# Optimization experiments

Hardware: AMD Instinct MI355X
Metric: run time of the kernel (lower is better)

The kernel has to match this reference:

```python
import jax, jax.numpy as jnp
import numpy as np

B, T, C = 8, 2048, 768
HEAD = 64
NUM_REL = 2048


def setup_inputs() -> dict:
    key = jax.random.key(0)
    k1, k2, k3, k4, k5 = jax.random.split(key, 5)
    input_tensor = jax.random.normal(k1, (B, T, C), dtype=jnp.float32)
    # torch Linear(C, HEAD, bias=False): y = x @ W.T, W:[HEAD,C]; store as [C,HEAD]
    Wq = jax.random.normal(k2, (C, HEAD), dtype=jnp.float32) * (C ** -0.5)
    Wk = jax.random.normal(k3, (C, HEAD), dtype=jnp.float32) * (C ** -0.5)
    Wv = jax.random.normal(k4, (C, HEAD), dtype=jnp.float32) * (C ** -0.5)
    bias_table = jax.random.normal(k5, (NUM_REL, 1), dtype=jnp.float32)
    return {"input_tensor": input_tensor, "Wq": Wq, "Wk": Wk, "Wv": Wv, "bias_table": bias_table}


def reference(input_tensor, Wq, Wk, Wv, bias_table):
    Bsz, Tlen, _ = input_tensor.shape
    q = input_tensor @ Wq  # [B,T,H]
    k = input_tensor @ Wk
    v = input_tensor @ Wv
    scale = q.shape[-1] ** -0.5
    scores = jnp.einsum('bqh,bkh->bqk', q, k) * scale  # [B,T,T]
    # relative position bias: clamp(i - j, 0, NUM_REL-1)
    qpos = jnp.arange(Tlen)[:, None]
    kpos = jnp.arange(Tlen)[None, :]
    rel = jnp.clip(qpos - kpos, 0, bias_table.shape[0] - 1)
    bias = bias_table[rel, 0]  # [T,T]
    scores = scores + bias
    causal = kpos <= qpos  # True where allowed
    scores = jnp.where(causal, scores, -jnp.inf)
    attn = jax.nn.softmax(scores, axis=-1)
    return jnp.einsum('bqk,bkh->bqh', attn, v)
```

## Files before the change

### kernel.cpp

```cpp
#include <hip/hip_runtime.h>
#include <hip/hip_bf16.h>

typedef __attribute__((ext_vector_type(8))) short bf16x8;
typedef __attribute__((ext_vector_type(4))) short short4v;
typedef __attribute__((ext_vector_type(4))) float f32x4;

#define B_SZ 8
#define T_SZ 2048
#define C_SZ 768
#define H_SZ 64

__device__ __forceinline__ short f2bs(float f){
  __hip_bfloat16 h = __float2bfloat16(f);
  short s; __builtin_memcpy(&s, &h, 2); return s;
}
__device__ __forceinline__ f32x4 vmax4(f32x4 a, f32x4 b){
  f32x4 r; r[0]=fmaxf(a[0],b[0]); r[1]=fmaxf(a[1],b[1]);
  r[2]=fmaxf(a[2],b[2]); r[3]=fmaxf(a[3],b[3]); return r;
}
__device__ __forceinline__ void gload16(const void* g, void* l){
  __builtin_amdgcn_global_load_lds(
    (const __attribute__((address_space(1))) unsigned int*)g,
    (__attribute__((address_space(3))) unsigned int*)l, 16, 0, 0);
}

__global__ __launch_bounds__(256) void prep_wt(const float* __restrict__ Wq, const float* __restrict__ Wk,
                        const float* __restrict__ Wv, const float* __restrict__ bias,
                        short* __restrict__ Wt, float* __restrict__ bsc){
  int tid = threadIdx.x;
  if (blockIdx.x >= 36){
    int i = (blockIdx.x - 36)*256 + tid;
    bsc[i] = bias[i] * 1.44269504f;
    return;
  }
  __shared__ float tile[64][65];
  int mat = blockIdx.x / 12, kblk = blockIdx.x % 12;
  const float* W = (mat == 0) ? Wq : (mat == 1 ? Wk : Wv);
  int k0 = kblk * 64;
  int r = tid >> 2, cq = (tid & 3) * 16;
  #pragma unroll
  for (int i = 0; i < 4; ++i){
    float4 v = *reinterpret_cast<const float4*>(&W[(k0 + r)*H_SZ + cq + i*4]);
    tile[r][cq + i*4 + 0] = v.x; tile[r][cq + i*4 + 1] = v.y;
    tile[r][cq + i*4 + 2] = v.z; tile[r][cq + i*4 + 3] = v.w;
  }
  __syncthreads();
  int n = tid >> 2, kq = (tid & 3) * 16;
  bf16x8 o0, o1;
  #pragma unroll
  for (int e = 0; e < 8; ++e){
    o0[e] = f2bs(tile[kq + e][n]);
    o1[e] = f2bs(tile[kq + 8 + e][n]);
  }
  *reinterpret_cast<bf16x8*>(&Wt[(mat*64 + n)*C_SZ + k0 + kq])     = o0;
  *reinterpret_cast<bf16x8*>(&Wt[(mat*64 + n)*C_SZ + k0 + kq + 8]) = o1;
}

__global__ __launch_bounds__(512, 2) void qkv_gemm(const float* __restrict__ x, const short* __restrict__ Wt,
                         short* __restrict__ qb, short* __restrict__ kb, short* __restrict__ vT){
  __shared__ float As[2][2048];
  __shared__ short Bs[2][12288];
  int tid = threadIdx.x;
  int wv = tid >> 6, lane = tid & 63, lhi = lane >> 4, llo = lane & 15;
  int wm = wv >> 2, wn = wv & 3;
  long R0 = (long)blockIdx.x * 32;

  int srow = tid >> 4;
  int schunk = (tid & 15) ^ (srow & 7);
  const float* gsrcA = &x[(R0 + srow)*C_SZ + schunk*4];
  float* ldstA = &As[0][wv*256];

  int bn = tid >> 3;
  int bc = (tid & 7) ^ (bn & 7);
  const short* gsrcB0 = &Wt[(  0 + bn)*C_SZ + bc*8];
  const short* gsrcB1 = &Wt[( 64 + bn)*C_SZ + bc*8];
  const short* gsrcB2 = &Wt[(128 + bn)*C_SZ + bc*8];
  short* ldstB = &Bs[0][wv*512];

  f32x4 acc[3];
  #pragma unroll
  for (int j = 0; j < 3; ++j) acc[j] = (f32x4){0.f,0.f,0.f,0.f};

  int rr = wm*16 + llo;
  int r7 = rr & 7, lhi2 = lhi*2;
  int c0 = ((lhi2    ) ^ r7) << 2;
  int c1 = ((lhi2 + 1) ^ r7) << 2;
  int c2 = ((lhi2 + 8) ^ r7) << 2;
  int c3 = ((lhi2 + 9) ^ r7) << 2;
  int nrow[3];
  #pragma unroll
  for (int j = 0; j < 3; ++j) nrow[j] = (wn*48 + j*16 + llo)*64;
  int llo7 = llo & 7;
  int bo0 = ((    lhi) ^ llo7)*8;
  int bo1 = ((4 + lhi) ^ llo7)*8;

#define STAGE(T, BUF) { \
    gload16(gsrcA  + (T)*64, ldstA + (BUF)*2048); \
    gload16(gsrcB0 + (T)*64, ldstB + (BUF)*12288); \
    gload16(gsrcB1 + (T)*64, ldstB + (BUF)*12288 + 4096); \
    gload16(gsrcB2 + (T)*64, ldstB + (BUF)*12288 + 8192); }

  STAGE(0, 0);
  __syncthreads();

  for (int t = 0; t < 12; ++t){
    int cb = t & 1;
    if (t < 11) STAGE(t + 1, cb ^ 1);
    const float* Ar = &As[cb][rr*64];
    f32x4 a0 = *reinterpret_cast<const f32x4*>(Ar + c0);
    f32x4 a1 = *reinterpret_cast<const f32x4*>(Ar + c1);
    f32x4 a2 = *reinterpret_cast<const f32x4*>(Ar + c2);
    f32x4 a3 = *reinterpret_cast<const f32x4*>(Ar + c3);
    bf16x8 af0, af1;
    #pragma unroll
    for (int e = 0; e < 4; ++e){
      af0[e]   = f2bs(a0[e]); af0[4+e] = f2bs(a1[e]);
      af1[e]   = f2bs(a2[e]); af1[4+e] = f2bs(a3[e]);
    }
    const short* Br = &Bs[cb][0];
    #pragma unroll
    for (int j = 0; j < 3; ++j){
      bf16x8 b0 = *reinterpret_cast<const bf16x8*>(Br + nrow[j] + bo0);
      bf16x8 b1 = *reinterpret_cast<const bf16x8*>(Br + nrow[j] + bo1);
      acc[j] = __builtin_amdgcn_mfma_f32_16x16x32_bf16(af0, b0, acc[j], 0, 0, 0);
      acc[j] = __builtin_amdgcn_mfma_f32_16x16x32_bf16(af1, b1, acc[j], 0, 0, 0);
    }
    __syncthreads();
  }
#undef STAGE

  long mbase = R0 + wm*16 + lhi*4;
  #pragma unroll
  for (int j = 0; j < 3; ++j){
    int n = wn*48 + j*16 + llo;
    int mat = n >> 6, c = n & 63;
    if (mat == 2){
      long b = mbase >> 11, t = mbase & 2047;
      short4v p;
      #pragma unroll
      for (int reg = 0; reg < 4; ++reg) p[reg] = f2bs(acc[j][reg]);
      *reinterpret_cast<short4v*>(&vT[(b*H_SZ + c)*T_SZ + t]) = p;
    } else {
      short* dst = (mat == 0) ? qb : kb;
      #pragma unroll
      for (int reg = 0; reg < 4; ++reg)
        dst[(mbase + reg)*H_SZ + c] = f2bs(acc[j][reg]);
    }
  }
}

__global__ __launch_bounds__(512, 2) void attn_fwd(const short* __restrict__ qb, const short* __restrict__ kb,
                        const short* __restrict__ vT, const float* __restrict__ bsc,
                        float* __restrict__ out){
  __shared__ float bias_s[2048];
  __shared__ float pool[8][1040];
  __shared__ float m_part[8][16];
  __shared__ float l_part[8][16];

  int tid = threadIdx.x;
  for (int i = tid; i < 2048; i += 512) bias_s[i] = bsc[i];

  int wv = tid >> 6, lane = tid & 63, lhi = lane >> 4, llo = lane & 15;
  int g = wv >> 2, ws = wv & 3;
  int b = blockIdx.x & 7, jj = blockIdx.x >> 3;
  int qt = g ? (127 - jj) : jj;
  int q0 = qt * 16;
  int q = q0 + llo;

  const short* qrow = &qb[((long)(b*T_SZ + q))*H_SZ + lhi*8];
  bf16x8 qf0 = *reinterpret_cast<const bf16x8*>(qrow);
  bf16x8 qf1 = *reinterpret_cast<const bf16x8*>(qrow + 32);
  const short* kbase = kb + (long)b*T_SZ*H_SZ;
  const short* vbase = vT + (long)b*H_SZ*T_SZ;
  short* Pw = (short*)&pool[wv][0];
  __syncthreads();

  float m_r = -1e30f, l_r = 0.f;
  f32x4 o[4];
  #pragma unroll
  for (int df = 0; df < 4; ++df) o[df] = (f32x4){0.f,0.f,0.f,0.f};

  int nkt = (qt >> 2) + 1;
  for (int kt = ws; kt < nkt; kt += 4){
    int kv0 = kt * 64;
    bf16x8 kf0[4], kf1[4];
    #pragma unroll
    for (int f = 0; f < 4; ++f){
      const short* kr = kbase + (long)(kv0 + f*16 + llo)*H_SZ + lhi*8;
      kf0[f] = *reinterpret_cast<const bf16x8*>(kr);
      kf1[f] = *reinterpret_cast<const bf16x8*>(kr + 32);
    }
    f32x4 s[4];
    #pragma unroll
    for (int f = 0; f < 4; ++f){
      f32x4 t = (f32x4){0.f,0.f,0.f,0.f};
      t = __builtin_amdgcn_mfma_f32_16x16x32_bf16(kf0[f], qf0, t, 0, 0, 0);
      t = __builtin_amdgcn_mfma_f32_16x16x32_bf16(kf1[f], qf1, t, 0, 0, 0);
      s[f] = t;
    }
    bf16x8 vf0[4], vf1[4];
    #pragma unroll
    for (int d = 0; d < 4; ++d){
      const short* vr = vbase + (long)(d*16 + llo)*T_SZ + kv0 + lhi*8;
      vf0[d] = *reinterpret_cast<const bf16x8*>(vr);
      vf1[d] = *reinterpret_cast<const bf16x8*>(vr + 32);
    }
    #pragma unroll
    for (int f = 0; f < 4; ++f)
      #pragma unroll
      for (int rg = 0; rg < 4; ++rg){
        int kv = kv0 + f*16 + lhi*4 + rg;
        int rel = q - kv;
        float bv = bias_s[rel > 0 ? rel : 0];
        s[f][rg] = (rel >= 0) ? fmaf(s[f][rg], 0.18033688f, bv) : -1e30f;
      }
    f32x4 tm = vmax4(vmax4(s[0], s[1]), vmax4(s[2], s[3]));
    float pmax = fmaxf(fmaxf(tm[0], tm[1]), fmaxf(tm[2], tm[3]));
    pmax = fmaxf(pmax, __shfl_xor(pmax, 16));
    pmax = fmaxf(pmax, __shfl_xor(pmax, 32));
    bool keep = __all(pmax <= m_r + 8.0f);
    if (!keep){
      float mnew = fmaxf(m_r, pmax);
      float corr = exp2f(m_r - mnew);
      m_r = mnew;
      l_r *= corr;
      #pragma unroll
      for (int df = 0; df < 4; ++df) o[df] = o[df] * corr;
    }
    #pragma unroll
    for (int f = 0; f < 4; ++f)
      #pragma unroll
      for (int rg = 0; rg < 4; ++rg)
        s[f][rg] = exp2f(s[f][rg] - m_r);
    f32x4 va = (s[0] + s[1]) + (s[2] + s[3]);
    float rs = (va[0] + va[1]) + (va[2] + va[3]);
    rs += __shfl_xor(rs, 16);
    rs += __shfl_xor(rs, 32);
    l_r += rs;
    #pragma unroll
    for (int f = 0; f < 4; ++f){
      short4v pk;
      #pragma unroll
      for (int rg = 0; rg < 4; ++rg) pk[rg] = f2bs(s[f][rg]);
      *reinterpret_cast<short4v*>(&Pw[llo*72 + f*16 + lhi*4]) = pk;
    }
    bf16x8 pb0 = *reinterpret_cast<const bf16x8*>(&Pw[llo*72 + lhi*8]);
    bf16x8 pb1 = *reinterpret_cast<const bf16x8*>(&Pw[llo*72 + 32 + lhi*8]);
    #pragma unroll
    for (int df = 0; df < 4; ++df){
      o[df] = __builtin_amdgcn_mfma_f32_16x16x32_bf16(vf0[df], pb0, o[df], 0, 0, 0);
      o[df] = __builtin_amdgcn_mfma_f32_16x16x32_bf16(vf1[df], pb1, o[df], 0, 0, 0);
    }
  }

  #pragma unroll
  for (int df = 0; df < 4; ++df)
    #pragma unroll
    for (int rg = 0; rg < 4; ++rg)
      pool[wv][llo*65 + df*16 + lhi*4 + rg] = o[df][rg];
  if (lhi == 0){ m_part[wv][llo] = m_r; l_part[wv][llo] = l_r; }
  __syncthreads();

  int g2 = tid >> 8, r2 = tid & 255;
  int d = r2 & 63, q4 = r2 >> 6;
  int qt2 = g2 ? (127 - jj) : jj;
  long obase = ((long)(b*T_SZ + qt2*16))*H_SZ;
  #pragma unroll
  for (int i = 0; i < 4; ++i){
    int qq = q4*4 + i;
    float mstar = m_part[g2*4][qq];
    #pragma unroll
    for (int w = 1; w < 4; ++w) mstar = fmaxf(mstar, m_part[g2*4 + w][qq]);
    float lsum = 0.f, osum = 0.f;
    #pragma unroll
    for (int w = 0; w < 4; ++w){
      float sc = exp2f(m_part[g2*4 + w][qq] - mstar);
      lsum += l_part[g2*4 + w][qq] * sc;
      osum += pool[g2*4 + w][qq*65 + d] * sc;
    }
    out[obase + (long)qq*H_SZ + d] = osum / lsum;
  }
}

extern "C" void kernel_launch(void* const* d_in, const int* in_sizes, int n_in,
                              void* d_out, int out_size, void* d_ws, size_t ws_size,
                              hipStream_t stream){
  const float* x    = (const float*)d_in[0];
  const float* Wq   = (const float*)d_in[1];
  const float* Wk   = (const float*)d_in[2];
  const float* Wv   = (const float*)d_in[3];
  const float* bias = (const float*)d_in[4];
  float* out = (float*)d_out;

  const size_t NTOK = (size_t)B_SZ * T_SZ * H_SZ;
  short* qb = (short*)d_ws;
  short* kb = qb + NTOK;
  short* vT = kb + NTOK;
  short* Wt = vT + NTOK;
  float* bsc = (float*)(Wt + 192*C_SZ);

  prep_wt<<<44, 256, 0, stream>>>(Wq, Wk, Wv, bias, Wt, bsc);
  qkv_gemm<<<512, 512, 0, stream>>>(x, Wt, qb, kb, vT);
  attn_fwd<<<512, 512, 0, stream>>>(qb, kb, vT, bsc, out);
}
```

Measured before the change: 62.32 us.

## Process paired query tiles in every wave, sharing K/V loads across both tiles

Each wave now computes both the light (jj) and heavy (127-jj) query tiles together, so every K and V fragment loaded is used for two MFMA streams instead of one. All 8 waves split the key range of the longer tile, which replaces the earlier fixed 4+4 wave split and spreads the causal work more evenly. The row-sum shuffles are deferred to the final merge by keeping per-lane partial sums, and launch bounds ask for 4 blocks per CU. The cost is extra accumulator registers, which may spill under the tighter register limit, plus two serialized merge passes with added block barriers.

```diff
diff --git a/kernel.cpp b/kernel.cpp
--- a/kernel.cpp
+++ b/kernel.cpp
@@ -149,137 +149,137 @@
   }
 }
 
-__global__ __launch_bounds__(512, 2) void attn_fwd(const short* __restrict__ qb, const short* __restrict__ kb,
+__global__ __launch_bounds__(512, 4) void attn_fwd(const short* __restrict__ qb, const short* __restrict__ kb,
                         const short* __restrict__ vT, const float* __restrict__ bsc,
                         float* __restrict__ out){
   __shared__ float bias_s[2048];
-  __shared__ float pool[8][1040];
+  __shared__ short P_lds[8][2][1152];
   __shared__ float m_part[8][16];
-  __shared__ float l_part[8][16];
+  __shared__ float l_part[8][4][16];
+  float* OP = (float*)&P_lds[0][0][0];
 
   int tid = threadIdx.x;
   for (int i = tid; i < 2048; i += 512) bias_s[i] = bsc[i];
 
   int wv = tid >> 6, lane = tid & 63, lhi = lane >> 4, llo = lane & 15;
-  int g = wv >> 2, ws = wv & 3;
   int b = blockIdx.x & 7, jj = blockIdx.x >> 3;
-  int qt = g ? (127 - jj) : jj;
-  int q0 = qt * 16;
-  int q = q0 + llo;
-
-  const short* qrow = &qb[((long)(b*T_SZ + q))*H_SZ + lhi*8];
-  bf16x8 qf0 = *reinterpret_cast<const bf16x8*>(qrow);
-  bf16x8 qf1 = *reinterpret_cast<const bf16x8*>(qrow + 32);
+  int qtA = jj, qtB = 127 - jj;
+  int qA = qtA*16 + llo, qB = qtB*16 + llo;
+  int nktA = (qtA >> 2) + 1, nktB = (qtB >> 2) + 1;
+
+  const short* qrA = &qb[((long)(b*T_SZ + qA))*H_SZ + lhi*8];
+  const short* qrB = &qb[((long)(b*T_SZ + qB))*H_SZ + lhi*8];
+  bf16x8 qfA0 = *reinterpret_cast<const bf16x8*>(qrA);
+  bf16x8 qfA1 = *reinterpret_cast<const bf16x8*>(qrA + 32);
+  bf16x8 qfB0 = *reinterpret_cast<const bf16x8*>(qrB);
+  bf16x8 qfB1 = *reinterpret_cast<const bf16x8*>(qrB + 32);
   const short* kbase = kb + (long)b*T_SZ*H_SZ;
   const short* vbase = vT + (long)b*H_SZ*T_SZ;
-  short* Pw = (short*)&pool[wv][0];
   __syncthreads();
 
-  float m_r = -1e30f, l_r = 0.f;
-  f32x4 o[4];
-  #pragma unroll
-  for (int df = 0; df < 4; ++df) o[df] = (f32x4){0.f,0.f,0.f,0.f};
-
-  int nkt = (qt >> 2) + 1;
-  for (int kt = ws; kt < nkt; kt += 4){
-    int kv0 = kt * 64;
-    bf16x8 kf0[4], kf1[4];
+  float mA = -1e30f, lA = 0.f, mB = -1e30f, lB = 0.f;
+  f32x4 oA[4], oB[4];
+  #pragma unroll
+  for (int df = 0; df < 4; ++df){ oA[df] = (f32x4){0.f,0.f,0.f,0.f}; oB[df] = (f32x4){0.f,0.f,0.f,0.f}; }
+
+#define SM(S, M, L, O, QV, TI, PB0, PB1) {                                  \
+    _Pragma("unroll") for (int f = 0; f < 4; ++f)                           \
+      _Pragma("unroll") for (int rg = 0; rg < 4; ++rg){                     \
+        int kv = kv0 + f*16 + lhi*4 + rg;                                   \
+        int rel = (QV) - kv;                                                \
+        float bv = bias_s[rel > 0 ? rel : 0];                               \
+        S[f][rg] = (rel >= 0) ? fmaf(S[f][rg], 0.18033688f, bv) : -1e30f; } \
+    f32x4 tm = vmax4(vmax4(S[0], S[1]), vmax4(S[2], S[3]));                 \
+    float pmax = fmaxf(fmaxf(tm[0], tm[1]), fmaxf(tm[2], tm[3]));           \
+    if (!__all(pmax <= M + 8.0f)){                                          \
+      float rm = fmaxf(pmax, __shfl_xor(pmax, 16));                         \
+      rm = fmaxf(rm, __shfl_xor(rm, 32));                                   \
+      float mnew = fmaxf(M, rm);                                            \
+      float corr = exp2f(M - mnew);                                         \
+      M = mnew; L *= corr;                                                  \
+      _Pragma("unroll") for (int df = 0; df < 4; ++df) O[df] = O[df]*corr; }\
+    _Pragma("unroll") for (int f = 0; f < 4; ++f){                          \
+      short4v pk;                                                           \
+      _Pragma("unroll") for (int rg = 0; rg < 4; ++rg){                     \
+        float p = exp2f(S[f][rg] - M); S[f][rg] = p; pk[rg] = f2bs(p); }    \
+      *reinterpret_cast<short4v*>(&P_lds[wv][TI][llo*72 + f*16 + lhi*4]) = pk; } \
+    f32x4 va = (S[0] + S[1]) + (S[2] + S[3]);                               \
+    L += (va[0] + va[1]) + (va[2] + va[3]);                                 \
+    PB0 = *reinterpret_cast<const bf16x8*>(&P_lds[wv][TI][llo*72 + lhi*8]); \
+    PB1 = *reinterpret_cast<const bf16x8*>(&P_lds[wv][TI][llo*72 + 32 + lhi*8]); }
+
+  for (int c = wv; c < nktB; c += 8){
+    int kv0 = c * 64;
+    bool doA = c < nktA;
+    f32x4 sA[4], sB[4];
     #pragma unroll
     for (int f = 0; f < 4; ++f){
       const short* kr = kbase + (long)(kv0 + f*16 + llo)*H_SZ + lhi*8;
-      kf0[f] = *reinterpret_cast<const bf16x8*>(kr);
-      kf1[f] = *reinterpret_cast<const bf16x8*>(kr + 32);
-    }
-    f32x4 s[4];
-    #pragma unroll
-    for (int f = 0; f < 4; ++f){
+      bf16x8 k0 = *reinterpret_cast<const bf16x8*>(kr);
+      bf16x8 k1 = *reinterpret_cast<const bf16x8*>(kr + 32);
       f32x4 t = (f32x4){0.f,0.f,0.f,0.f};
-      t = __builtin_amdgcn_mfma_f32_16x16x32_bf16(kf0[f], qf0, t, 0, 0, 0);
-      t = __builtin_amdgcn_mfma_f32_16x16x32_bf16(kf1[f], qf1, t, 0, 0, 0);
-      s[f] = t;
-    }
-    bf16x8 vf0[4], vf1[4];
-    #pragma unroll
-    for (int d = 0; d < 4; ++d){
-      const short* vr = vbase + (long)(d*16 + llo)*T_SZ + kv0 + lhi*8;
-      vf0[d] = *reinterpret_cast<const bf16x8*>(vr);
-      vf1[d] = *reinterpret_cast<const bf16x8*>(vr + 32);
-    }
-    #pragma unroll
-    for (int f = 0; f < 4; ++f)
+      t = __builtin_amdgcn_mfma_f32_16x16x32_bf16(k0, qfB0, t, 0, 0, 0);
+      t = __builtin_amdgcn_mfma_f32_16x16x32_bf16(k1, qfB1, t, 0, 0, 0);
+      sB[f] = t;
+      f32x4 u = (f32x4){0.f,0.f,0.f,0.f};
+      u = __builtin_amdgcn_mfma_f32_16x16x32_bf16(k0, qfA0, u, 0, 0, 0);
+      u = __builtin_amdgcn_mfma_f32_16x16x32_bf16(k1, qfA1, u, 0, 0, 0);
+      sA[f] = u;
+    }
+    bf16x8 pbB0, pbB1;
+    SM(sB, mB, lB, oB, qB, 1, pbB0, pbB1);
+    if (doA){
+      bf16x8 pbA0, pbA1;
+      SM(sA, mA, lA, oA, qA, 0, pbA0, pbA1);
       #pragma unroll
-      for (int rg = 0; rg < 4; ++rg){
-        int kv = kv0 + f*16 + lhi*4 + rg;
-        int rel = q - kv;
-        float bv = bias_s[rel > 0 ? rel : 0];
-        s[f][rg] = (rel >= 0) ? fmaf(s[f][rg], 0.18033688f, bv) : -1e30f;
+      for (int df = 0; df < 4; ++df){
+        const short* vr = vbase + (long)(df*16 + llo)*T_SZ + kv0 + lhi*8;
+        bf16x8 v0 = *reinterpret_cast<const bf16x8*>(vr);
+        bf16x8 v1 = *reinterpret_cast<const bf16x8*>(vr + 32);
+        oB[df] = __builtin_amdgcn_mfma_f32_16x16x32_bf16(v0, pbB0, oB[df], 0, 0, 0);
+        oB[df] = __builtin_amdgcn_mfma_f32_16x16x32_bf16(v1, pbB1, oB[df], 0, 0, 0);
+        oA[df] = __builtin_amdgcn_mfma_f32_16x16x32_bf16(v0, pbA0, oA[df], 0, 0, 0);
+        oA[df] = __builtin_amdgcn_mfma_f32_16x16x32_bf16(v1, pbA1, oA[df], 0, 0, 0);
       }
-    f32x4 tm = vmax4(vmax4(s[0], s[1]), vmax4(s[2], s[3]));
-    float pmax = fmaxf(fmaxf(tm[0], tm[1]), fmaxf(tm[2], tm[3]));
-    pmax = fmaxf(pmax, __shfl_xor(pmax, 16));
-    pmax = fmaxf(pmax, __shfl_xor(pmax, 32));
-    bool keep = __all(pmax <= m_r + 8.0f);
-    if (!keep){
-      float mnew = fmaxf(m_r, pmax);
-      float corr = exp2f(m_r - mnew);
-      m_r = mnew;
-      l_r *= corr;
+    } else {
       #pragma unroll
-      for (int df = 0; df < 4; ++df) o[df] = o[df] * corr;
-    }
-    #pragma unroll
-    for (int f = 0; f < 4; ++f)
-      #pragma unroll
-      for (int rg = 0; rg < 4; ++rg)
-        s[f][rg] = exp2f(s[f][rg] - m_r);
-    f32x4 va = (s[0] + s[1]) + (s[2] + s[3]);
-    float rs = (va[0] + va[1]) + (va[2] + va[3]);
-    rs += __shfl_xor(rs, 16);
-    rs += __shfl_xor(rs, 32);
-    l_r += rs;
-    #pragma unroll
-    for (int f = 0; f < 4; ++f){
-      short4v pk;
-      #pragma unroll
-      for (int rg = 0; rg < 4; ++rg) pk[rg] = f2bs(s[f][rg]);
-      *reinterpret_cast<short4v*>(&Pw[llo*72 + f*16 + lhi*4]) = pk;
-    }
-    bf16x8 pb0 = *reinterpret_cast<const bf16x8*>(&Pw[llo*72 + lhi*8]);
-    bf16x8 pb1 = *reinterpret_cast<const bf16x8*>(&Pw[llo*72 + 32 + lhi*8]);
-    #pragma unroll
-    for (int df = 0; df < 4; ++df){
-      o[df] = __builtin_amdgcn_mfma_f32_16x16x32_bf16(vf0[df], pb0, o[df], 0, 0, 0);
-      o[df] = __builtin_amdgcn_mfma_f32_16x16x32_bf16(vf1[df], pb1, o[df], 0, 0, 0);
-    }
-  }
-
-  #pragma unroll
-  for (int df = 0; df < 4; ++df)
-    #pragma unroll
-    for (int rg = 0; rg < 4; ++rg)
-      pool[wv][llo*65 + df*16 + lhi*4 + rg] = o[df][rg];
-  if (lhi == 0){ m_part[wv][llo] = m_r; l_part[wv][llo] = l_r; }
-  __syncthreads();
-
-  int g2 = tid >> 8, r2 = tid & 255;
-  int d = r2 & 63, q4 = r2 >> 6;
-  int qt2 = g2 ? (127 - jj) : jj;
-  long obase = ((long)(b*T_SZ + qt2*16))*H_SZ;
-  #pragma unroll
-  for (int i = 0; i < 4; ++i){
-    int qq = q4*4 + i;
-    float mstar = m_part[g2*4][qq];
-    #pragma unroll
-    for (int w = 1; w < 4; ++w) mstar = fmaxf(mstar, m_part[g2*4 + w][qq]);
-    float lsum = 0.f, osum = 0.f;
-    #pragma unroll
-    for (int w = 0; w < 4; ++w){
-      float sc = exp2f(m_part[g2*4 + w][qq] - mstar);
-      lsum += l_part[g2*4 + w][qq] * sc;
-      osum += pool[g2*4 + w][qq*65 + d] * sc;
-    }
-    out[obase + (long)qq*H_SZ + d] = osum / lsum;
-  }
+      for (int df = 0; df < 4; ++df){
+        const short* vr = vbase + (long)(df*16 + llo)*T_SZ + kv0 + lhi*8;
+        bf16x8 v0 = *reinterpret_cast<const bf16x8*>(vr);
+        bf16x8 v1 = *reinterpret_cast<const bf16x8*>(vr + 32);
+        oB[df] = __builtin_amdgcn_mfma_f32_16x16x32_bf16(v0, pbB0, oB[df], 0, 0, 0);
+        oB[df] = __builtin_amdgcn_mfma_f32_16x16x32_bf16(v1, pbB1, oB[df], 0, 0, 0);
+      }
+    }
+  }
+#undef SM
+
+#define MERGE(O, M, L, QT) {                                                \
+    _Pragma("unroll") for (int df = 0; df < 4; ++df)                        \
+      _Pragma("unroll") for (int rg = 0; rg < 4; ++rg)                      \
+        OP[wv*1152 + llo*65 + df*16 + lhi*4 + rg] = O[df][rg];              \
+    l_part[wv][lhi][llo] = L;                                               \
+    if (lhi == 0) m_part[wv][llo] = M;                                      \
+    __syncthreads();                                                        \
+    { int idx = tid;                                                        \
+      _Pragma("unroll") for (int rep = 0; rep < 2; ++rep){                  \
+        int row = idx >> 6, d = idx & 63;                                   \
+        float mstar = m_part[0][row];                                       \
+        _Pragma("unroll") for (int w = 1; w < 8; ++w)                       \
+          mstar = fmaxf(mstar, m_part[w][row]);                             \
+        float lsum = 0.f, osum = 0.f;                                       \
+        _Pragma("unroll") for (int w = 0; w < 8; ++w){                      \
+          float sc = exp2f(m_part[w][row] - mstar);                         \
+          lsum += sc * (l_part[w][0][row] + l_part[w][1][row]               \
+                      + l_part[w][2][row] + l_part[w][3][row]);             \
+          osum += sc * OP[w*1152 + row*65 + d]; }                           \
+        out[((long)(b*T_SZ + (QT)*16 + row))*H_SZ + d] = osum / lsum;       \
+        idx += 512; } }                                                     \
+    __syncthreads(); }
+
+  MERGE(oB, mB, lB, qtB);
+  MERGE(oA, mA, lA, qtA);
+#undef MERGE
 }
 
 extern "C" void kernel_launch(void* const* d_in, const int* in_sizes, int n_in,
```

After: 58.33 us, median of 2. 1.07x faster.

## Split each attention block to one query tile across eight KV-split waves

Applied to the files above, without the earlier changes.

Each attention block now handles a single 16-row query tile, with all eight waves splitting its KV range, instead of pairing two tiles with four waves each. The grid doubles to 1024 blocks, and a smaller LDS footprint plus launch_bounds(512,8) aim for higher occupancy. The row-sum shuffle is deferred to a per-lane partial reduced in the final merge, and V loads are moved next to their MFMAs to cut register pressure. The cost is an 8-way merge done in two halves through reused LDS with extra barriers, and short causal rows leave most waves idle.

```diff
diff --git a/kernel.cpp b/kernel.cpp
--- a/kernel.cpp
+++ b/kernel.cpp
@@ -149,30 +149,31 @@
   }
 }
 
-__global__ __launch_bounds__(512, 2) void attn_fwd(const short* __restrict__ qb, const short* __restrict__ kb,
+__global__ __launch_bounds__(512, 8) void attn_fwd(const short* __restrict__ qb, const short* __restrict__ kb,
                         const short* __restrict__ vT, const float* __restrict__ bsc,
                         float* __restrict__ out){
   __shared__ float bias_s[2048];
-  __shared__ float pool[8][1040];
+  __shared__ short P_lds[8][1152];
   __shared__ float m_part[8][16];
-  __shared__ float l_part[8][16];
+  __shared__ float l_part[8][4][16];
+  float* OP = (float*)&P_lds[0][0];
 
   int tid = threadIdx.x;
   for (int i = tid; i < 2048; i += 512) bias_s[i] = bsc[i];
 
   int wv = tid >> 6, lane = tid & 63, lhi = lane >> 4, llo = lane & 15;
-  int g = wv >> 2, ws = wv & 3;
-  int b = blockIdx.x & 7, jj = blockIdx.x >> 3;
-  int qt = g ? (127 - jj) : jj;
+  int b = blockIdx.x & 7;
+  int qt = 127 - (blockIdx.x >> 3);
   int q0 = qt * 16;
   int q = q0 + llo;
+  int nkt = (qt >> 2) + 1;
 
   const short* qrow = &qb[((long)(b*T_SZ + q))*H_SZ + lhi*8];
   bf16x8 qf0 = *reinterpret_cast<const bf16x8*>(qrow);
   bf16x8 qf1 = *reinterpret_cast<const bf16x8*>(qrow + 32);
   const short* kbase = kb + (long)b*T_SZ*H_SZ;
   const short* vbase = vT + (long)b*H_SZ*T_SZ;
-  short* Pw = (short*)&pool[wv][0];
+  short* Pw = &P_lds[wv][0];
   __syncthreads();
 
   float m_r = -1e30f, l_r = 0.f;
@@ -180,30 +181,18 @@
   #pragma unroll
   for (int df = 0; df < 4; ++df) o[df] = (f32x4){0.f,0.f,0.f,0.f};
 
-  int nkt = (qt >> 2) + 1;
-  for (int kt = ws; kt < nkt; kt += 4){
-    int kv0 = kt * 64;
-    bf16x8 kf0[4], kf1[4];
+  for (int c = wv; c < nkt; c += 8){
+    int kv0 = c * 64;
+    f32x4 s[4];
     #pragma unroll
     for (int f = 0; f < 4; ++f){
       const short* kr = kbase + (long)(kv0 + f*16 + llo)*H_SZ + lhi*8;
-      kf0[f] = *reinterpret_cast<const bf16x8*>(kr);
-      kf1[f] = *reinterpret_cast<const bf16x8*>(kr + 32);
-    }
-    f32x4 s[4];
-    #pragma unroll
-    for (int f = 0; f < 4; ++f){
+      bf16x8 k0 = *reinterpret_cast<const bf16x8*>(kr);
+      bf16x8 k1 = *reinterpret_cast<const bf16x8*>(kr + 32);
       f32x4 t = (f32x4){0.f,0.f,0.f,0.f};
-      t = __builtin_amdgcn_mfma_f32_16x16x32_bf16(kf0[f], qf0, t, 0, 0, 0);
-      t = __builtin_amdgcn_mfma_f32_16x16x32_bf16(kf1[f], qf1, t, 0, 0, 0);
+      t = __builtin_amdgcn_mfma_f32_16x16x32_bf16(k0, qf0, t, 0, 0, 0);
+      t = __builtin_amdgcn_mfma_f32_16x16x32_bf16(k1, qf1, t, 0, 0, 0);
       s[f] = t;
-    }
-    bf16x8 vf0[4], vf1[4];
-    #pragma unroll
-    for (int d = 0; d < 4; ++d){
-      const short* vr = vbase + (long)(d*16 + llo)*T_SZ + kv0 + lhi*8;
-      vf0[d] = *reinterpret_cast<const bf16x8*>(vr);
-      vf1[d] = *reinterpret_cast<const bf16x8*>(vr + 32);
     }
     #pragma unroll
     for (int f = 0; f < 4; ++f)
@@ -216,69 +205,68 @@
       }
     f32x4 tm = vmax4(vmax4(s[0], s[1]), vmax4(s[2], s[3]));
     float pmax = fmaxf(fmaxf(tm[0], tm[1]), fmaxf(tm[2], tm[3]));
-    pmax = fmaxf(pmax, __shfl_xor(pmax, 16));
-    pmax = fmaxf(pmax, __shfl_xor(pmax, 32));
-    bool keep = __all(pmax <= m_r + 8.0f);
-    if (!keep){
-      float mnew = fmaxf(m_r, pmax);
+    if (!__all(pmax <= m_r + 8.0f)){
+      float rm = fmaxf(pmax, __shfl_xor(pmax, 16));
+      rm = fmaxf(rm, __shfl_xor(rm, 32));
+      float mnew = fmaxf(m_r, rm);
       float corr = exp2f(m_r - mnew);
-      m_r = mnew;
-      l_r *= corr;
+      m_r = mnew; l_r *= corr;
       #pragma unroll
       for (int df = 0; df < 4; ++df) o[df] = o[df] * corr;
     }
-    #pragma unroll
-    for (int f = 0; f < 4; ++f)
-      #pragma unroll
-      for (int rg = 0; rg < 4; ++rg)
-        s[f][rg] = exp2f(s[f][rg] - m_r);
-    f32x4 va = (s[0] + s[1]) + (s[2] + s[3]);
-    float rs = (va[0] + va[1]) + (va[2] + va[3]);
-    rs += __shfl_xor(rs, 16);
-    rs += __shfl_xor(rs, 32);
-    l_r += rs;
     #pragma unroll
     for (int f = 0; f < 4; ++f){
       short4v pk;
       #pragma unroll
-      for (int rg = 0; rg < 4; ++rg) pk[rg] = f2bs(s[f][rg]);
+      for (int rg = 0; rg < 4; ++rg){
+        float p = exp2f(s[f][rg] - m_r);
+        s[f][rg] = p; pk[rg] = f2bs(p);
+      }
       *reinterpret_cast<short4v*>(&Pw[llo*72 + f*16 + lhi*4]) = pk;
     }
+    f32x4 va = (s[0] + s[1]) + (s[2] + s[3]);
+    l_r += (va[0] + va[1]) + (va[2] + va[3]);
     bf16x8 pb0 = *reinterpret_cast<const bf16x8*>(&Pw[llo*72 + lhi*8]);
     bf16x8 pb1 = *reinterpret_cast<const bf16x8*>(&Pw[llo*72 + 32 + lhi*8]);
     #pragma unroll
     for (int df = 0; df < 4; ++df){
-      o[df] = __builtin_amdgcn_mfma_f32_16x16x32_bf16(vf0[df], pb0, o[df], 0, 0, 0);
-      o[df] = __builtin_amdgcn_mfma_f32_16x16x32_bf16(vf1[df], pb1, o[df], 0, 0, 0);
-    }
-  }
-
-  #pragma unroll
-  for (int df = 0; df < 4; ++df)
-    #pragma unroll
-    for (int rg = 0; rg < 4; ++rg)
-      pool[wv][llo*65 + df*16 + lhi*4 + rg] = o[df][rg];
-  if (lhi == 0){ m_part[wv][llo] = m_r; l_part[wv][llo] = l_r; }
-  __syncthreads();
-
-  int g2 = tid >> 8, r2 = tid & 255;
-  int d = r2 & 63, q4 = r2 >> 6;
-  int qt2 = g2 ? (127 - jj) : jj;
-  long obase = ((long)(b*T_SZ + qt2*16))*H_SZ;
-  #pragma unroll
-  for (int i = 0; i < 4; ++i){
-    int qq = q4*4 + i;
-    float mstar = m_part[g2*4][qq];
-    #pragma unroll
-    for (int w = 1; w < 4; ++w) mstar = fmaxf(mstar, m_part[g2*4 + w][qq]);
-    float lsum = 0.f, osum = 0.f;
-    #pragma unroll
-    for (int w = 0; w < 4; ++w){
-      float sc = exp2f(m_part[g2*4 + w][qq] - mstar);
-      lsum += l_part[g2*4 + w][qq] * sc;
-      osum += pool[g2*4 + w][qq*65 + d] * sc;
-    }
-    out[obase + (long)qq*H_SZ + d] = osum / lsum;
+      const short* vr = vbase + (long)(df*16 + llo)*T_SZ + kv0 + lhi*8;
+      bf16x8 v0 = *reinterpret_cast<const bf16x8*>(vr);
+      bf16x8 v1 = *reinterpret_cast<const bf16x8*>(vr + 32);
+      o[df] = __builtin_amdgcn_mfma_f32_16x16x32_bf16(v0, pb0, o[df], 0, 0, 0);
+      o[df] = __builtin_amdgcn_mfma_f32_16x16x32_bf16(v1, pb1, o[df], 0, 0, 0);
+    }
+  }
+
+  l_part[wv][lhi][llo] = l_r;
+  if (lhi == 0) m_part[wv][llo] = m_r;
+  long obase = ((long)(b*T_SZ + q0))*H_SZ;
+  #pragma unroll
+  for (int h = 0; h < 2; ++h){
+    #pragma unroll
+    for (int dh = 0; dh < 2; ++dh){
+      int df = h*2 + dh;
+      #pragma unroll
+      for (int rg = 0; rg < 4; ++rg)
+        OP[wv*576 + llo*36 + dh*16 + lhi*4 + rg] = o[df][rg];
+    }
+    __syncthreads();
+    {
+      int row = tid >> 5, dcol = tid & 31;
+      float mstar = m_part[0][row];
+      #pragma unroll
+      for (int w = 1; w < 8; ++w) mstar = fmaxf(mstar, m_part[w][row]);
+      float lsum = 0.f, osum = 0.f;
+      #pragma unroll
+      for (int w = 0; w < 8; ++w){
+        float sc = exp2f(m_part[w][row] - mstar);
+        lsum += sc * (l_part[w][0][row] + l_part[w][1][row]
+                    + l_part[w][2][row] + l_part[w][3][row]);
+        osum += sc * OP[w*576 + row*36 + dcol];
+      }
+      out[obase + (long)row*H_SZ + h*32 + dcol] = osum / lsum;
+    }
+    __syncthreads();
   }
 }
 
@@ -301,5 +289,5 @@
 
   prep_wt<<<44, 256, 0, stream>>>(Wq, Wk, Wv, bias, Wt, bsc);
   qkv_gemm<<<512, 512, 0, stream>>>(x, Wt, qb, kb, vT);
-  attn_fwd<<<512, 512, 0, stream>>>(qb, kb, vT, bsc, out);
-}
+  attn_fwd<<<1024, 512, 0, stream>>>(qb, kb, vT, bsc, out);
+}
```

Result: slower. 76.23 us (+22.3%).
